# Kernel optimization log

Measured on AMD Instinct MI355X. Metric: run time of the kernel, lower is better.

## Reference

```python
import jax, jax.numpy as jnp
import numpy as np

H = 16
LN_EPS = 1e-5


def setup_inputs() -> dict:
    key = jax.random.key(0)
    ks = jax.random.split(key, 8)
    B, N, D = 2, 2048, 1024
    s = D ** -0.5
    return {
        "q_s": jax.random.normal(ks[0], (B, N, D), jnp.float32),
        "pos_emb": jax.random.normal(ks[1], (B, N, D), jnp.float32),
        "Wq": jax.random.normal(ks[2], (D, D), jnp.float32) * s,
        "Wk": jax.random.normal(ks[3], (D, D), jnp.float32) * s,
        "Wv": jax.random.normal(ks[4], (D, D), jnp.float32) * s,
        "Wo": jax.random.normal(ks[5], (D, D), jnp.float32) * s,
        "bo": jnp.zeros((D,), jnp.float32),
        "ln_g": jnp.ones((D,), jnp.float32),
        "ln_b": jnp.zeros((D,), jnp.float32),
    }


def _split_heads(t):
    b, n, d = t.shape
    return t.reshape(b, n, H, d // H).transpose(0, 2, 1, 3)  # b h n d


def reference(q_s, pos_emb, Wq, Wk, Wv, Wo, bo, ln_g, ln_b):
    # self-attention: k_s = v_s = q_s
    q = _split_heads(q_s @ Wq)
    k = _split_heads(q_s @ Wk)
    v = _split_heads(q_s @ Wv)
    p = _split_heads(pos_emb)
    scale = q.shape[-1] ** -0.5
    # content-content + content-position attention logits: [b,h,i,j]
    att = (jnp.einsum('bhid,bhjd->bhij', q, k) + jnp.einsum('bhid,bhjd->bhij', q, p)) * scale
    att = jax.nn.softmax(att, axis=-1)
    o = jnp.einsum('bhij,bhjd->bhid', att, v)
    b, h, n, d = o.shape
    o = o.transpose(0, 2, 1, 3).reshape(b, n, h * d)
    o = o @ Wo + bo  # out_layer (dropout rate 0 -> identity)
    x = o + q_s  # residual
    mu = jnp.mean(x, axis=-1, keepdims=True)
    var = jnp.var(x, axis=-1, keepdims=True)
    return (x - mu) * jax.lax.rsqrt(var + LN_EPS) * ln_g + ln_b
```

## Files before the change

kernel.cpp:

```cpp
#include <hip/hip_runtime.h>
#include <hip/hip_bf16.h>
#include <stdint.h>

typedef unsigned short u16;
typedef unsigned int u32;
typedef short s16x8 __attribute__((ext_vector_type(8)));
typedef short s16x4 __attribute__((ext_vector_type(4)));
typedef float f32x4 __attribute__((ext_vector_type(4)));

#define MFMA(a, b, c) __builtin_amdgcn_mfma_f32_16x16x32_bf16((a), (b), (c), 0, 0, 0)

__device__ __forceinline__ float bf2f(u16 h) {
  u32 u = ((u32)h) << 16;
  float f;
  __builtin_memcpy(&f, &u, 4);
  return f;
}

__device__ __forceinline__ u16 f2bf_rte(float f) {
  __hip_bfloat16 h = __float2bfloat16(f);
  u16 u;
  __builtin_memcpy(&u, &h, 2);
  return u;
}

__device__ __forceinline__ void gload16(const u16* g, u16* l) {
  __builtin_amdgcn_global_load_lds((const __attribute__((address_space(1))) u32*)g,
                                   (__attribute__((address_space(3))) u32*)l, 16, 0, 0);
}

__global__ __launch_bounds__(256) void k_cvt(const float* __restrict__ in,
                                             u16* __restrict__ out, int n8) {
  int i = blockIdx.x * 256 + threadIdx.x;
  if (i >= n8) return;
  const f32x4* p = (const f32x4*)(in + (size_t)i * 8);
  f32x4 a = p[0], b = p[1];
  s16x8 o;
  for (int k = 0; k < 4; ++k) o[k] = (short)f2bf_rte(a[k]);
  for (int k = 0; k < 4; ++k) o[4 + k] = (short)f2bf_rte(b[k]);
  *(s16x8*)(out + (size_t)i * 8) = o;
}

__global__ __launch_bounds__(256) void k_prep_pos(const float* __restrict__ pos,
                                                  u16* __restrict__ Pp) {
  const int t = threadIdx.x;
  const int bh = blockIdx.y, b = bh >> 4, h = bh & 15;
  const int n = blockIdx.x * 64 + (t >> 2);
  const int d0 = (t & 3) * 16;
  const float* src = &pos[((size_t)(b * 2048 + n)) * 1024 + h * 64 + d0];
  u16* dst = &Pp[((size_t)bh * 2048 + n) * 64 + d0];
  f32x4 a = *(const f32x4*)src;
  f32x4 bq = *(const f32x4*)(src + 4);
  f32x4 c = *(const f32x4*)(src + 8);
  f32x4 dq = *(const f32x4*)(src + 12);
  s16x8 o0, o1;
  for (int i = 0; i < 4; ++i) {
    o0[i] = (short)f2bf_rte(a[i]);
    o0[4 + i] = (short)f2bf_rte(bq[i]);
    o1[i] = (short)f2bf_rte(c[i]);
    o1[4 + i] = (short)f2bf_rte(dq[i]);
  }
  *(s16x8*)dst = o0;
  *(s16x8*)(dst + 8) = o1;
}

__global__ __launch_bounds__(256) void k_transpose_w(const float* __restrict__ W0,
                                                     const float* __restrict__ W1,
                                                     const float* __restrict__ W2,
                                                     const float* __restrict__ W3,
                                                     u16* __restrict__ out) {
  const int z = blockIdx.z;
  const float* in = (z == 0) ? W0 : (z == 1) ? W1 : (z == 2) ? W2 : W3;
  u16* o = out + (size_t)z * 1024 * 1024;
  __shared__ u16 tile[64][65];
  const int t = threadIdx.x, tx = t & 63, ty = t >> 6;
  const int r0 = blockIdx.y * 64, c0 = blockIdx.x * 64;
  for (int rr = 0; rr < 16; ++rr) {
    int row = rr * 4 + ty;
    tile[row][tx] = f2bf_rte(in[(size_t)(r0 + row) * 1024 + c0 + tx]);
  }
  __syncthreads();
  for (int rr = 0; rr < 16; ++rr) {
    int row = rr * 4 + ty;
    o[(size_t)(c0 + row) * 1024 + r0 + tx] = tile[tx][row];
  }
}

__global__ __launch_bounds__(256) void k_transpose_v(const u16* __restrict__ V,
                                                     u16* __restrict__ Vt) {
  __shared__ u16 tile[64][65];
  const int t = threadIdx.x, tx = t & 63, ty = t >> 6;
  const int j0 = blockIdx.x * 64;
  const int bh = blockIdx.y;
  const u16* src = V + (size_t)bh * 2048 * 64;
  u16* dst = Vt + (size_t)bh * 64 * 2048;
  for (int rr = 0; rr < 16; ++rr) {
    int row = rr * 4 + ty;
    tile[row][tx] = src[(size_t)(j0 + row) * 64 + tx];
  }
  __syncthreads();
  for (int rr = 0; rr < 16; ++rr) {
    int d = rr * 4 + ty;
    dst[(size_t)d * 2048 + j0 + tx] = tile[tx][d];
  }
}

__global__ __launch_bounds__(256) void k_qkv_gemm(const u16* __restrict__ X,
                                                  const u16* __restrict__ WT,
                                                  const u16* __restrict__ Pp,
                                                  u16* __restrict__ Qh,
                                                  u16* __restrict__ Kh,
                                                  u16* __restrict__ Vh) {
  __shared__ u16 As[3][4096];
  __shared__ u16 Bs[3][4096];
  const int t = threadIdx.x;
  const int lane = t & 63, wid = t >> 6;
  const int wr = wid >> 1, wc = wid & 1;
  const int g = lane >> 4, lr = lane & 15;
  const int lin = blockIdx.y * 24 + blockIdx.x;
  const int swz = (lin & 7) * 96 + (lin >> 3);
  const int m0 = (swz / 24) * 128, n0 = (swz % 24) * 128;

  const int srcRow = t >> 2;
  const int srcKsw = ((t & 3) * 8) ^ (((t >> 3) & 3) << 3);
  const u16* aSrc = &X[(size_t)(m0 + srcRow) * 1024 + srcKsw];
  const u16* bSrc = &WT[(size_t)(n0 + srcRow) * 1024 + srcKsw];

  const int csw = (g * 8) ^ (((lr >> 1) & 3) << 3);

  f32x4 acc[4][4] = {};

#define QKV_STAGE(buf, k0)                                   \
  {                                                          \
    gload16(aSrc + (k0), &As[buf][wid * 512]);               \
    gload16(aSrc + 65536 + (k0), &As[buf][wid * 512 + 2048]);\
    gload16(bSrc + (k0), &Bs[buf][wid * 512]);               \
    gload16(bSrc + 65536 + (k0), &Bs[buf][wid * 512 + 2048]);\
  }

  QKV_STAGE(0, 0);
  QKV_STAGE(1, 32);
  QKV_STAGE(2, 64);
  for (int k = 0; k < 32; ++k) {
    if (k < 30) {
      asm volatile("s_waitcnt vmcnt(8)" ::: "memory");
    } else if (k == 30) {
      asm volatile("s_waitcnt vmcnt(4)" ::: "memory");
    } else {
      asm volatile("s_waitcnt vmcnt(0)" ::: "memory");
    }
    __builtin_amdgcn_sched_barrier(0);
    __builtin_amdgcn_s_barrier();
    const int cur = k % 3;
    s16x8 a[4], b[4];
#pragma unroll
    for (int mi = 0; mi < 4; ++mi)
      a[mi] = *(const s16x8*)&As[cur][(wr * 64 + mi * 16 + lr) * 32 + csw];
#pragma unroll
    for (int nj = 0; nj < 4; ++nj)
      b[nj] = *(const s16x8*)&Bs[cur][(wc * 64 + nj * 16 + lr) * 32 + csw];
#pragma unroll
    for (int mi = 0; mi < 4; ++mi)
#pragma unroll
      for (int nj = 0; nj < 4; ++nj)
        acc[mi][nj] = MFMA(a[mi], b[nj], acc[mi][nj]);
    __builtin_amdgcn_s_barrier();
    if (k < 29) QKV_STAGE(cur, (k + 3) * 32);
  }
#undef QKV_STAGE

  const float QSCALE = 0.125f * 1.44269504f;
  for (int mi = 0; mi < 4; ++mi) {
    for (int nj = 0; nj < 4; ++nj) {
      const int n_g = n0 + wc * 64 + nj * 16 + lr;
      const int buf = n_g >> 10;
      const int col = n_g & 1023;
      const int h = col >> 6, d = col & 63;
      u16* dst = (buf == 0) ? Qh : ((buf == 1) ? Kh : Vh);
      for (int r = 0; r < 4; ++r) {
        const int row = m0 + wr * 64 + mi * 16 + g * 4 + r;
        const int b = row >> 11, n = row & 2047;
        const size_t off = (size_t)((b * 16 + h) * 2048 + n) * 64 + d;
        float v = acc[mi][nj][r];
        if (buf == 1) v += bf2f(Pp[off]);
        if (buf == 0) v *= QSCALE;
        dst[off] = f2bf_rte(v);
      }
    }
  }
}

__global__ __launch_bounds__(512, 4) void k_attn(const u16* __restrict__ Qh,
                                                 const u16* __restrict__ Kh,
                                                 const u16* __restrict__ Vt,
                                                 u16* __restrict__ Oh) {
  const int t = threadIdx.x, lane = t & 63, wid = t >> 6;
  const int g = lane >> 4, lr = lane & 15;
  const int hid = blockIdx.x;
  const int lid = (hid & 7) * 64 + (hid >> 3);
  const int bh = lid >> 4, itile = lid & 15;
  const int i0 = itile * 128 + wid * 16;

  __shared__ char Ks[4][8192];
  __shared__ char Vs[4][8192];

  const u16* Qp = Qh + (size_t)bh * 2048 * 64;
  const u16* Kp = Kh + (size_t)bh * 2048 * 64;
  const u16* Vp = Vt + (size_t)bh * 64 * 2048;

  s16x8 aq[2];
  aq[0] = *(const s16x8*)&Qp[(size_t)(i0 + lr) * 64 + g * 8];
  aq[1] = *(const s16x8*)&Qp[(size_t)(i0 + lr) * 64 + 32 + g * 8];

  f32x4 oa[4] = {};
  float ms = -1e30f, ls = 0.f;

  const int srow = t >> 3;
  const int sch = (t & 7) * 16;
  const int schS = sch ^ ((srow & 7) << 4);
  const u16* kB = &Kp[(size_t)srow * 64 + (schS >> 1)];
  const u16* vB = &Vp[(size_t)srow * 2048 + (schS >> 1)];

#define ATTN_STAGE(p)                                                \
  {                                                                  \
    gload16(kB + (size_t)(p) * 4096, (u16*)Ks[(p) & 3] + wid * 512); \
    gload16(vB + (size_t)(p) * 64, (u16*)Vs[(p) & 3] + wid * 512);   \
  }

#define ATTN_BODY(BUF)                                                         \
  {                                                                            \
    const char* Kc = Ks[BUF];                                                  \
    const char* Vc = Vs[BUF];                                                  \
    f32x4 s[4] = {};                                                           \
    _Pragma("unroll") for (int jf = 0; jf < 4; ++jf) {                         \
      const int row = jf * 16 + lr;                                            \
      const int bw = (row & 7) << 4;                                           \
      s16x8 bk0 = *(const s16x8*)(Kc + ((row * 128 + g * 16) ^ bw));           \
      s16x8 bk1 = *(const s16x8*)(Kc + ((row * 128 + 64 + g * 16) ^ bw));      \
      s[jf] = MFMA(bk0, aq[0], s[jf]);                                         \
      s[jf] = MFMA(bk1, aq[1], s[jf]);                                         \
    }                                                                          \
                                                       \
    float mj[4];                                                               \
    _Pragma("unroll") for (int jf = 0; jf < 4; ++jf)                           \
        mj[jf] = fmaxf(fmaxf(s[jf][0], s[jf][1]), fmaxf(s[jf][2], s[jf][3]));  \
    float tl = fmaxf(fmaxf(mj[0], mj[1]), fmaxf(mj[2], mj[3]));                \
    if (!__all(tl <= ms + 8.f)) {                                              \
      float tm = fmaxf(tl, __shfl_xor(tl, 16, 64));                            \
      tm = fmaxf(tm, __shfl_xor(tm, 32, 64));                                  \
      float mn = fmaxf(ms, tm);                                                \
      float al = __builtin_amdgcn_exp2f(ms - mn);                              \
      ls *= al;                                                                \
      ms = mn;                                                                 \
      _Pragma("unroll") for (int r = 0; r < 4; ++r) {                          \
        float ab = __shfl(al, g * 4 + r, 64);                                  \
        _Pragma("unroll") for (int df = 0; df < 4; ++df) oa[df][r] *= ab;      \
      }                                                                        \
    }                                                                          \
                                            \
    float pj[4];                                                               \
    _Pragma("unroll") for (int jf = 0; jf < 4; ++jf) {                         \
      _Pragma("unroll") for (int r = 0; r < 4; ++r)                            \
          s[jf][r] = __builtin_amdgcn_exp2f(s[jf][r] - ms);                    \
      pj[jf] = (s[jf][0] + s[jf][1]) + (s[jf][2] + s[jf][3]);                  \
    }                                                                          \
    ls += (pj[0] + pj[1]) + (pj[2] + pj[3]);                                   \
    u32 pk[4][2];                                                              \
    _Pragma("unroll") for (int jf = 0; jf < 4; ++jf) {                         \
      asm("v_cvt_pk_bf16_f32 %0, %1, %2"                                       \
          : "=v"(pk[jf][0]) : "v"(s[jf][0]), "v"(s[jf][1]));                   \
      asm("v_cvt_pk_bf16_f32 %0, %1, %2"                                       \
          : "=v"(pk[jf][1]) : "v"(s[jf][2]), "v"(s[jf][3]));                   \
    }                                                                          \
    s16x8 pa[2];                                                               \
    _Pragma("unroll") for (int c = 0; c < 2; ++c) {                            \
      u32 w_[4];                                                               \
      _Pragma("unroll") for (int wl = 0; wl < 2; ++wl) {                       \
        u32 A = pk[2 * c][wl], B = pk[2 * c + 1][wl];                          \
        asm("v_permlane32_swap_b32 %0, %1" : "+v"(A), "+v"(B));                \
        asm("v_permlane16_swap_b32 %0, %1" : "+v"(A), "+v"(B));                \
        w_[wl] = A;                                                            \
        w_[2 + wl] = B;                                                        \
      }                                                                        \
      __builtin_memcpy(&pa[c], w_, 16);                                        \
    }                                                                          \
    _Pragma("unroll") for (int df = 0; df < 4; ++df) {                         \
      const int row = df * 16 + lr;                                            \
      const int bw = (row & 7) << 4;                                           \
      s16x8 bv0 = *(const s16x8*)(Vc + ((row * 128 + g * 16) ^ bw));           \
      s16x8 bv1 = *(const s16x8*)(Vc + ((row * 128 + 64 + g * 16) ^ bw));      \
      oa[df] = MFMA(pa[0], bv0, oa[df]);                                       \
      oa[df] = MFMA(pa[1], bv1, oa[df]);                                       \
    }                                                                          \
  }

  ATTN_STAGE(0);
  ATTN_STAGE(1);
  ATTN_STAGE(2);

  for (int tb = 0; tb < 7; ++tb) {
#pragma unroll
    for (int ti = 0; ti < 4; ++ti) {
      const int tt = tb * 4 + ti;
      asm volatile("s_waitcnt vmcnt(4)" ::: "memory");
      __builtin_amdgcn_sched_barrier(0);
      __builtin_amdgcn_s_barrier();
      ATTN_STAGE(tt + 3);
      ATTN_BODY(ti);
    }
  }
  {
    asm volatile("s_waitcnt vmcnt(4)" ::: "memory");
    __builtin_amdgcn_sched_barrier(0);
    __builtin_amdgcn_s_barrier();
    ATTN_STAGE(31);
    ATTN_BODY(0);
  }
  {
    asm volatile("s_waitcnt vmcnt(4)" ::: "memory");
    __builtin_amdgcn_sched_barrier(0);
    __builtin_amdgcn_s_barrier();
    ATTN_BODY(1);
  }
  {
    asm volatile("s_waitcnt vmcnt(2)" ::: "memory");
    __builtin_amdgcn_sched_barrier(0);
    __builtin_amdgcn_s_barrier();
    ATTN_BODY(2);
  }
  {
    asm volatile("s_waitcnt vmcnt(0)" ::: "memory");
    __builtin_amdgcn_sched_barrier(0);
    __builtin_amdgcn_s_barrier();
    ATTN_BODY(3);
  }
#undef ATTN_BODY
#undef ATTN_STAGE

  ls += __shfl_xor(ls, 16, 64);
  ls += __shfl_xor(ls, 32, 64);
  float lb[4];
#pragma unroll
  for (int r = 0; r < 4; ++r) lb[r] = __shfl(ls, g * 4 + r, 64);

  u16* Op = Oh + (size_t)bh * 2048 * 64;
#pragma unroll
  for (int df = 0; df < 4; ++df)
#pragma unroll
    for (int r = 0; r < 4; ++r) {
      const int row0 = i0 + g * 4 + r;
      Op[(size_t)row0 * 64 + df * 16 + lr] = f2bf_rte(oa[df][r] / lb[r]);
    }
}

__global__ __launch_bounds__(256) void k_out_gemm(const u16* __restrict__ Oh,
                                                  const u16* __restrict__ WTo,
                                                  const float* __restrict__ bo,
                                                  const u16* __restrict__ qsb,
                                                  float* __restrict__ X) {
  __shared__ u16 As[3][4096];
  __shared__ u16 Bs[3][4096];
  const int t = threadIdx.x;
  const int lane = t & 63, wid = t >> 6;
  const int wr = wid >> 1, wc = wid & 1;
  const int g = lane >> 4, lr = lane & 15;
  const int lin = blockIdx.y * 8 + blockIdx.x;
  const int swz = (lin & 7) * 32 + (lin >> 3);
  const int m0 = (swz / 8) * 128, n0 = (swz % 8) * 128;

  const int srcRow = t >> 2;
  const int srcKsw = ((t & 3) * 8) ^ (((t >> 3) & 3) << 3);
  const int rg = m0 + srcRow, bb0 = rg >> 11, nn0 = rg & 2047;
  const int rg2 = rg + 64, bb2 = rg2 >> 11, nn2 = rg2 & 2047;
  const u16* bSrc = &WTo[(size_t)(n0 + srcRow) * 1024 + srcKsw];
  const int csw = (g * 8) ^ (((lr >> 1) & 3) << 3);

  f32x4 acc[4][4] = {};

#define OUT_STAGE(buf, k0)                                                        \
  {                                                                               \
    const int h_ = (k0) >> 6, d_ = ((k0) & 63) + srcKsw;                          \
    gload16(&Oh[((size_t)(bb0 * 16 + h_) * 2048 + nn0) * 64 + d_],                \
            &As[buf][wid * 512]);                                                 \
    gload16(&Oh[((size_t)(bb2 * 16 + h_) * 2048 + nn2) * 64 + d_],                \
            &As[buf][wid * 512 + 2048]);                                          \
    gload16(bSrc + (k0), &Bs[buf][wid * 512]);                                    \
    gload16(bSrc + 65536 + (k0), &Bs[buf][wid * 512 + 2048]);                     \
  }

  OUT_STAGE(0, 0);
  OUT_STAGE(1, 32);
  OUT_STAGE(2, 64);
  for (int k = 0; k < 32; ++k) {
    if (k < 30) {
      asm volatile("s_waitcnt vmcnt(8)" ::: "memory");
    } else if (k == 30) {
      asm volatile("s_waitcnt vmcnt(4)" ::: "memory");
    } else {
      asm volatile("s_waitcnt vmcnt(0)" ::: "memory");
    }
    __builtin_amdgcn_sched_barrier(0);
    __builtin_amdgcn_s_barrier();
    const int cur = k % 3;
    s16x8 a[4], b[4];
#pragma unroll
    for (int mi = 0; mi < 4; ++mi)
      a[mi] = *(const s16x8*)&As[cur][(wr * 64 + mi * 16 + lr) * 32 + csw];
#pragma unroll
    for (int nj = 0; nj < 4; ++nj)
      b[nj] = *(const s16x8*)&Bs[cur][(wc * 64 + nj * 16 + lr) * 32 + csw];
#pragma unroll
    for (int mi = 0; mi < 4; ++mi)
#pragma unroll
      for (int nj = 0; nj < 4; ++nj)
        acc[mi][nj] = MFMA(a[mi], b[nj], acc[mi][nj]);
    __builtin_amdgcn_s_barrier();
    if (k < 29) OUT_STAGE(cur, (k + 3) * 32);
  }
#undef OUT_STAGE

  for (int mi = 0; mi < 4; ++mi) {
    for (int nj = 0; nj < 4; ++nj) {
      const int col = n0 + wc * 64 + nj * 16 + lr;
      for (int r = 0; r < 4; ++r) {
        const int row = m0 + wr * 64 + mi * 16 + g * 4 + r;
        float v = acc[mi][nj][r] + bo[col] + bf2f(qsb[(size_t)row * 1024 + col]);
        X[(size_t)row * 1024 + col] = v;
      }
    }
  }
}

__global__ __launch_bounds__(256) void k_ln(const float* __restrict__ X,
                                            const float* __restrict__ gg,
                                            const float* __restrict__ bb,
                                            float* __restrict__ out) {
  const int row = blockIdx.x, t = threadIdx.x;
  const int wid = t >> 6, lane = t & 63;
  const float* xr = X + (size_t)row * 1024;
  f32x4 x = *(const f32x4*)&xr[t * 4];
  float s1 = x[0] + x[1] + x[2] + x[3];
  float s2 = x[0] * x[0] + x[1] * x[1] + x[2] * x[2] + x[3] * x[3];
  for (int off = 32; off > 0; off >>= 1) {
    s1 += __shfl_down(s1, off, 64);
    s2 += __shfl_down(s2, off, 64);
  }
  __shared__ float red[2][4];
  if (lane == 0) { red[0][wid] = s1; red[1][wid] = s2; }
  __syncthreads();
  s1 = red[0][0] + red[0][1] + red[0][2] + red[0][3];
  s2 = red[1][0] + red[1][1] + red[1][2] + red[1][3];
  const float mu = s1 * (1.f / 1024.f);
  const float var = s2 * (1.f / 1024.f) - mu * mu;
  const float rstd = rsqrtf(var + 1e-5f);
  f32x4 gv = *(const f32x4*)&gg[t * 4];
  f32x4 bv = *(const f32x4*)&bb[t * 4];
  f32x4 ov;
  for (int i = 0; i < 4; ++i) ov[i] = (x[i] - mu) * rstd * gv[i] + bv[i];
  *(f32x4*)&out[(size_t)row * 1024 + t * 4] = ov;
}

extern "C" void kernel_launch(void* const* d_in, const int* in_sizes, int n_in,
                              void* d_out, int out_size, void* d_ws, size_t ws_size,
                              hipStream_t stream) {
  (void)in_sizes; (void)n_in; (void)out_size; (void)ws_size;
  const float* q_s = (const float*)d_in[0];
  const float* pos = (const float*)d_in[1];
  const float* Wq = (const float*)d_in[2];
  const float* Wk = (const float*)d_in[3];
  const float* Wv = (const float*)d_in[4];
  const float* Wo = (const float*)d_in[5];
  const float* bo = (const float*)d_in[6];
  const float* lng = (const float*)d_in[7];
  const float* lnb = (const float*)d_in[8];
  float* out = (float*)d_out;

  u16* ws = (u16*)d_ws;
  const size_t MB1 = 1024 * 1024;
  u16* WT  = ws;
  u16* Xbf = ws + 4 * MB1;
  u16* Qh  = Xbf + 4 * MB1;
  u16* Kh  = Qh + 4 * MB1;
  u16* Vh  = Kh + 4 * MB1;
  u16* Vt  = Vh + 4 * MB1;
  u16* Oh  = Vt + 4 * MB1;
  u16* Pp  = Oh;
  float* Xb = (float*)Qh;

  dim3 blk(256);
  k_cvt<<<dim3(2048), blk, 0, stream>>>(q_s, Xbf, 4 * MB1 / 8);
  k_prep_pos<<<dim3(32, 32), blk, 0, stream>>>(pos, Pp);
  k_transpose_w<<<dim3(16, 16, 4), blk, 0, stream>>>(Wq, Wk, Wv, Wo, WT);
  k_qkv_gemm<<<dim3(24, 32), blk, 0, stream>>>(Xbf, WT, Pp, Qh, Kh, Vh);
  k_transpose_v<<<dim3(32, 32), blk, 0, stream>>>(Vh, Vt);
  k_attn<<<dim3(512), dim3(512), 0, stream>>>(Qh, Kh, Vt, Oh);
  k_out_gemm<<<dim3(8, 32), blk, 0, stream>>>(Oh, WT + 3 * MB1, bo, Xbf, Xb);
  k_ln<<<4096, blk, 0, stream>>>(Xb, lng, lnb, out);
}
```

Measured before the change: 147.5 us.

## Merge prep kernels into one launch and use 4-stage single-barrier GEMM pipeline

Folds the three preprocessing kernels (activation conversion, positional-embedding repack, weight transpose) into a single launch that dispatches on block index, removing two kernel launches and their gaps. In both GEMMs the LDS ring grows from 3 to 4 buffers, so the next stage's prefetch is issued right after the top barrier and the second barrier per iteration is dropped. This raises LDS use per block, which may lower occupancy. The waitcnt thresholds were not adjusted for the new issue order.

```diff
diff --git a/kernel.cpp b/kernel.cpp
--- a/kernel.cpp
+++ b/kernel.cpp
@@ -29,60 +29,64 @@
                                    (__attribute__((address_space(3))) u32*)l, 16, 0, 0);
 }
 
-__global__ __launch_bounds__(256) void k_cvt(const float* __restrict__ in,
-                                             u16* __restrict__ out, int n8) {
-  int i = blockIdx.x * 256 + threadIdx.x;
-  if (i >= n8) return;
-  const f32x4* p = (const f32x4*)(in + (size_t)i * 8);
-  f32x4 a = p[0], b = p[1];
-  s16x8 o;
-  for (int k = 0; k < 4; ++k) o[k] = (short)f2bf_rte(a[k]);
-  for (int k = 0; k < 4; ++k) o[4 + k] = (short)f2bf_rte(b[k]);
-  *(s16x8*)(out + (size_t)i * 8) = o;
-}
-
-__global__ __launch_bounds__(256) void k_prep_pos(const float* __restrict__ pos,
-                                                  u16* __restrict__ Pp) {
+__global__ __launch_bounds__(256) void k_prep(const float* __restrict__ q_s,
+                                              const float* __restrict__ pos,
+                                              const float* __restrict__ W0,
+                                              const float* __restrict__ W1,
+                                              const float* __restrict__ W2,
+                                              const float* __restrict__ W3,
+                                              u16* __restrict__ Xbf,
+                                              u16* __restrict__ Pp,
+                                              u16* __restrict__ WT) {
+  __shared__ u16 tile[64][65];
+  const int b = blockIdx.x;
   const int t = threadIdx.x;
-  const int bh = blockIdx.y, b = bh >> 4, h = bh & 15;
-  const int n = blockIdx.x * 64 + (t >> 2);
-  const int d0 = (t & 3) * 16;
-  const float* src = &pos[((size_t)(b * 2048 + n)) * 1024 + h * 64 + d0];
-  u16* dst = &Pp[((size_t)bh * 2048 + n) * 64 + d0];
-  f32x4 a = *(const f32x4*)src;
-  f32x4 bq = *(const f32x4*)(src + 4);
-  f32x4 c = *(const f32x4*)(src + 8);
-  f32x4 dq = *(const f32x4*)(src + 12);
-  s16x8 o0, o1;
-  for (int i = 0; i < 4; ++i) {
-    o0[i] = (short)f2bf_rte(a[i]);
-    o0[4 + i] = (short)f2bf_rte(bq[i]);
-    o1[i] = (short)f2bf_rte(c[i]);
-    o1[4 + i] = (short)f2bf_rte(dq[i]);
-  }
-  *(s16x8*)dst = o0;
-  *(s16x8*)(dst + 8) = o1;
-}
-
-__global__ __launch_bounds__(256) void k_transpose_w(const float* __restrict__ W0,
-                                                     const float* __restrict__ W1,
-                                                     const float* __restrict__ W2,
-                                                     const float* __restrict__ W3,
-                                                     u16* __restrict__ out) {
-  const int z = blockIdx.z;
-  const float* in = (z == 0) ? W0 : (z == 1) ? W1 : (z == 2) ? W2 : W3;
-  u16* o = out + (size_t)z * 1024 * 1024;
-  __shared__ u16 tile[64][65];
-  const int t = threadIdx.x, tx = t & 63, ty = t >> 6;
-  const int r0 = blockIdx.y * 64, c0 = blockIdx.x * 64;
-  for (int rr = 0; rr < 16; ++rr) {
-    int row = rr * 4 + ty;
-    tile[row][tx] = f2bf_rte(in[(size_t)(r0 + row) * 1024 + c0 + tx]);
-  }
-  __syncthreads();
-  for (int rr = 0; rr < 16; ++rr) {
-    int row = rr * 4 + ty;
-    o[(size_t)(c0 + row) * 1024 + r0 + tx] = tile[tx][row];
+  if (b < 2048) {
+    const int i = b * 256 + t;
+    const f32x4* p = (const f32x4*)(q_s + (size_t)i * 8);
+    f32x4 a = p[0], bb = p[1];
+    s16x8 o;
+    for (int k = 0; k < 4; ++k) o[k] = (short)f2bf_rte(a[k]);
+    for (int k = 0; k < 4; ++k) o[4 + k] = (short)f2bf_rte(bb[k]);
+    *(s16x8*)(Xbf + (size_t)i * 8) = o;
+  } else if (b < 3072) {
+    const int pb = b - 2048;
+    const int bh = pb >> 5, bx = pb & 31;
+    const int bq = bh >> 4, h = bh & 15;
+    const int n = bx * 64 + (t >> 2);
+    const int d0 = (t & 3) * 16;
+    const float* src = &pos[((size_t)(bq * 2048 + n)) * 1024 + h * 64 + d0];
+    u16* dst = &Pp[((size_t)bh * 2048 + n) * 64 + d0];
+    f32x4 a = *(const f32x4*)src;
+    f32x4 bq4 = *(const f32x4*)(src + 4);
+    f32x4 c = *(const f32x4*)(src + 8);
+    f32x4 dq = *(const f32x4*)(src + 12);
+    s16x8 o0, o1;
+    for (int i = 0; i < 4; ++i) {
+      o0[i] = (short)f2bf_rte(a[i]);
+      o0[4 + i] = (short)f2bf_rte(bq4[i]);
+      o1[i] = (short)f2bf_rte(c[i]);
+      o1[4 + i] = (short)f2bf_rte(dq[i]);
+    }
+    *(s16x8*)dst = o0;
+    *(s16x8*)(dst + 8) = o1;
+  } else {
+    const int wb = b - 3072;
+    const int z = wb >> 8, r2 = wb & 255;
+    const int bx = r2 & 15, by = r2 >> 4;
+    const float* in = (z == 0) ? W0 : (z == 1) ? W1 : (z == 2) ? W2 : W3;
+    u16* o = WT + (size_t)z * 1024 * 1024;
+    const int tx = t & 63, ty = t >> 6;
+    const int r0 = by * 64, c0 = bx * 64;
+    for (int rr = 0; rr < 16; ++rr) {
+      int row = rr * 4 + ty;
+      tile[row][tx] = f2bf_rte(in[(size_t)(r0 + row) * 1024 + c0 + tx]);
+    }
+    __syncthreads();
+    for (int rr = 0; rr < 16; ++rr) {
+      int row = rr * 4 + ty;
+      o[(size_t)(c0 + row) * 1024 + r0 + tx] = tile[tx][row];
+    }
   }
 }
 
@@ -111,8 +115,8 @@
                                                   u16* __restrict__ Qh,
                                                   u16* __restrict__ Kh,
                                                   u16* __restrict__ Vh) {
-  __shared__ u16 As[3][4096];
-  __shared__ u16 Bs[3][4096];
+  __shared__ u16 As[4][4096];
+  __shared__ u16 Bs[4][4096];
   const int t = threadIdx.x;
   const int lane = t & 63, wid = t >> 6;
   const int wr = wid >> 1, wc = wid & 1;
@@ -151,7 +155,8 @@
     }
     __builtin_amdgcn_sched_barrier(0);
     __builtin_amdgcn_s_barrier();
-    const int cur = k % 3;
+    if (k < 29) QKV_STAGE((k + 3) & 3, (k + 3) * 32);
+    const int cur = k & 3;
     s16x8 a[4], b[4];
 #pragma unroll
     for (int mi = 0; mi < 4; ++mi)
@@ -164,8 +169,6 @@
 #pragma unroll
       for (int nj = 0; nj < 4; ++nj)
         acc[mi][nj] = MFMA(a[mi], b[nj], acc[mi][nj]);
-    __builtin_amdgcn_s_barrier();
-    if (k < 29) QKV_STAGE(cur, (k + 3) * 32);
   }
 #undef QKV_STAGE
 
@@ -240,7 +243,6 @@
       s[jf] = MFMA(bk0, aq[0], s[jf]);                                         \
       s[jf] = MFMA(bk1, aq[1], s[jf]);                                         \
     }                                                                          \
-                                                       \
     float mj[4];                                                               \
     _Pragma("unroll") for (int jf = 0; jf < 4; ++jf)                           \
         mj[jf] = fmaxf(fmaxf(s[jf][0], s[jf][1]), fmaxf(s[jf][2], s[jf][3]));  \
@@ -257,7 +259,6 @@
         _Pragma("unroll") for (int df = 0; df < 4; ++df) oa[df][r] *= ab;      \
       }                                                                        \
     }                                                                          \
-                                            \
     float pj[4];                                                               \
     _Pragma("unroll") for (int jf = 0; jf < 4; ++jf) {                         \
       _Pragma("unroll") for (int r = 0; r < 4; ++r)                            \
@@ -358,8 +359,8 @@
                                                   const float* __restrict__ bo,
                                                   const u16* __restrict__ qsb,
                                                   float* __restrict__ X) {
-  __shared__ u16 As[3][4096];
-  __shared__ u16 Bs[3][4096];
+  __shared__ u16 As[4][4096];
+  __shared__ u16 Bs[4][4096];
   const int t = threadIdx.x;
   const int lane = t & 63, wid = t >> 6;
   const int wr = wid >> 1, wc = wid & 1;
@@ -401,7 +402,8 @@
     }
     __builtin_amdgcn_sched_barrier(0);
     __builtin_amdgcn_s_barrier();
-    const int cur = k % 3;
+    if (k < 29) OUT_STAGE((k + 3) & 3, (k + 3) * 32);
+    const int cur = k & 3;
     s16x8 a[4], b[4];
 #pragma unroll
     for (int mi = 0; mi < 4; ++mi)
@@ -414,8 +416,6 @@
 #pragma unroll
       for (int nj = 0; nj < 4; ++nj)
         acc[mi][nj] = MFMA(a[mi], b[nj], acc[mi][nj]);
-    __builtin_amdgcn_s_barrier();
-    if (k < 29) OUT_STAGE(cur, (k + 3) * 32);
   }
 #undef OUT_STAGE
 
@@ -488,9 +488,7 @@
   float* Xb = (float*)Qh;
 
   dim3 blk(256);
-  k_cvt<<<dim3(2048), blk, 0, stream>>>(q_s, Xbf, 4 * MB1 / 8);
-  k_prep_pos<<<dim3(32, 32), blk, 0, stream>>>(pos, Pp);
-  k_transpose_w<<<dim3(16, 16, 4), blk, 0, stream>>>(Wq, Wk, Wv, Wo, WT);
+  k_prep<<<dim3(4096), blk, 0, stream>>>(q_s, pos, Wq, Wk, Wv, Wo, Xbf, Pp, WT);
   k_qkv_gemm<<<dim3(24, 32), blk, 0, stream>>>(Xbf, WT, Pp, Qh, Kh, Vh);
   k_transpose_v<<<dim3(32, 32), blk, 0, stream>>>(Vh, Vt);
   k_attn<<<dim3(512), dim3(512), 0, stream>>>(Qh, Kh, Vt, Oh);
```

After: 157.9 us. 7.0% more time.
